# Performance work log

Hardware: AMD Instinct MI355X
Metric: run time of the kernel (lower is better)

## Reference

```python
import jax, jax.numpy as jnp
import numpy as np

B, T, L = 512, 512, 128  # batch, seq_len, tag-vocab size (incl. START=126, STOP=127)


def setup_inputs() -> dict:
    key = jax.random.key(0)
    k1, k2, k3 = jax.random.split(key, 3)
    # scale emissions so exp(gold path score) stays finite in fp32
    feats = jax.random.normal(k1, (B, T, L), dtype=jnp.float32) * 0.05
    # xavier_normal on [L, L] -> std = sqrt(2/(L+L)) = 1/sqrt(L)
    transfer = jax.random.normal(k2, (L, L), dtype=jnp.float32) * (1.0 / np.sqrt(L))
    target = jax.random.randint(k3, (B, T), 0, L - 2, dtype=jnp.int32)
    return {"feats": feats, "transfer": transfer, "target": target,
            "start": L - 2, "stop": L - 1}


def _crf_loss(feats, transfer, target, start, stop):
    # feats: [B, T, L] emissions; transfer: [L, L]; target: [B, T] gold tags
    Bb, Tt, Ll = feats.shape

    # ---- forward algorithm (log-sum-exp DP over tags) ----
    # scores[1] = feats[1] + transfer[start, :]
    prev0 = feats[:, 1] + transfer[start][None, :]  # [B, L]

    def step(prev, f_t):
        # original: scores[t, y] = LSE_x( scores[t-1, x] + feats[t, x] + transfer[x, y] )
        v = prev + f_t                                        # [B, L] over prev-tag x
        new = jax.nn.logsumexp(v[:, :, None] + transfer[None, :, :], axis=1)  # [B, L]
        return new, None

    step = jax.checkpoint(step)  # keep scan residuals to just the carries
    feats_rest = jnp.swapaxes(feats[:, 2:], 0, 1)  # [T-2, B, L]
    prev, _ = jax.lax.scan(step, prev0, feats_rest)
    sentence_score = jax.nn.logsumexp(prev + transfer[:, stop][None, :], axis=1)  # [B]

    # ---- gold path score ----
    emit0 = feats[:, 0, start]  # hh[0, start]
    emit = jnp.take_along_axis(feats[:, 1:], target[:, 1:, None], axis=2)[..., 0].sum(axis=1)
    pre = jnp.concatenate(
        [jnp.full((Bb, 1), start, dtype=target.dtype), target[:, 1:Tt - 1]], axis=1)  # [B, T-1]
    # original reads transfer[pre, tgt].data[0] -> detached constant
    trans = jax.lax.stop_gradient(transfer[pre, target[:, 1:]]).sum(axis=1)
    gold_score = jnp.exp(emit0 + emit + trans)  # original returns torch.exp(score)

    return sentence_score - gold_score  # per-sentence loss, shape [B]


def reference(feats, transfer, target, start, stop):
    return _crf_loss(feats, transfer, target, start, stop)
```

## Files before the change

kernel.cpp:

```cpp
#include <hip/hip_runtime.h>

#define T_DIM 512
#define L_DIM 128

typedef _Float16 h2 __attribute__((ext_vector_type(2)));

#if defined(__has_builtin)
#if __has_builtin(__builtin_amdgcn_fdot2)
#define HAS_FDOT2 1
#endif
#endif

__device__ __forceinline__ float fdot2_acc(h2 a, h2 b, float c) {
#ifdef HAS_FDOT2
    return __builtin_amdgcn_fdot2(a, b, c, false);
#else
    return c + (float)a.x * (float)b.x + (float)a.y * (float)b.y;
#endif
}

__device__ __forceinline__ unsigned int pack_u32(float a, float b) {
    return __builtin_bit_cast(unsigned int, __builtin_amdgcn_cvt_pkrtz(a, b));
}

#define H2C(x) __builtin_bit_cast(h2, (x))

__device__ __forceinline__ void lds_barrier() {
    asm volatile("s_waitcnt lgkmcnt(0)\n\ts_barrier" ::: "memory");
}


#define E_GROUPS(X) X(0) X(1) X(2) X(3) X(4) X(5) X(6) X(7) \
                    X(8) X(9) X(10) X(11) X(12) X(13) X(14) X(15)

__global__ __launch_bounds__(128, 1) void crf_fwd_kernel(
    const float* __restrict__ feats,
    const float* __restrict__ transfer,
    const int* __restrict__ target,
    const int* __restrict__ startp,
    const int* __restrict__ stopp,
    float* __restrict__ out)
{
    __shared__ unsigned int LdsU[2][64] __attribute__((aligned(16)));
    __shared__ float LdsRed[8];

    const int tid  = threadIdx.x;
    const int lane = tid & 63;
    const int wv   = tid >> 6;
    const int g    = tid;
    const int b    = blockIdx.x;
    const int start = startp[0];
    const int stop  = stopp[0];
    const float* fbase = feats + (size_t)b * T_DIM * L_DIM;
    const float LOG128 = 4.852030263919617f;
    const float SCALE  = 0.0078125f;

#define DECL_E(v) uint4 E##v;
    E_GROUPS(DECL_E)
#undef DECL_E

#define LDT(r) transfer[(r) * L_DIM + g]
#define LOAD_E(v) { \
    float e0 = __expf(LDT(8*(v)+0)) * SCALE, e1 = __expf(LDT(8*(v)+1)) * SCALE; \
    float e2 = __expf(LDT(8*(v)+2)) * SCALE, e3 = __expf(LDT(8*(v)+3)) * SCALE; \
    float e4 = __expf(LDT(8*(v)+4)) * SCALE, e5 = __expf(LDT(8*(v)+5)) * SCALE; \
    float e6 = __expf(LDT(8*(v)+6)) * SCALE, e7 = __expf(LDT(8*(v)+7)) * SCALE; \
    E##v.x = pack_u32(e0, e1); E##v.y = pack_u32(e2, e3); \
    E##v.z = pack_u32(e4, e5); E##v.w = pack_u32(e6, e7); }
    E_GROUPS(LOAD_E)
#undef LOAD_E
#undef LDT

    const float trStop = transfer[g * L_DIM + stop];

    {
        float v2 = fbase[1 * L_DIM + g] + fbase[2 * L_DIM + g]
                 + transfer[start * L_DIM + g];
        _Float16 h = (_Float16)__expf(v2);
        reinterpret_cast<unsigned short*>(&LdsU[0][0])[g] =
            __builtin_bit_cast(unsigned short, h);
    }
    float fa = fbase[3 * L_DIM + g];
    float fb = fbase[4 * L_DIM + g];
    float fc = fbase[5 * L_DIM + g];
    float S  = 0.f;
    lds_barrier();

    int cur = 0;
    float accF = 0.f;

    for (int t = 2; t <= T_DIM - 1; ++t) {
        int tp = t + 4; if (tp > T_DIM - 1) tp = T_DIM - 1;
        float fnew = fbase[tp * L_DIM + g];
        float e = __expf(fa);

        if ((t & 15) == 0) {
            h2 h = H2C(LdsU[cur][0]);
            float u0 = (float)h.x;
            e *= 1.0f / u0;
            S += __logf(u0);
        }

        const uint4* U4p = reinterpret_cast<const uint4*>(&LdsU[cur][0]);
        float s0 = 0.f, s1 = 0.f, s2 = 0.f, s3 = 0.f;

#define DOT_G(v, AC) { \
        uint4 p = U4p[v]; \
        AC = fdot2_acc(H2C(p.x), H2C(E##v.x), AC); \
        AC = fdot2_acc(H2C(p.y), H2C(E##v.y), AC); \
        AC = fdot2_acc(H2C(p.z), H2C(E##v.z), AC); \
        AC = fdot2_acc(H2C(p.w), H2C(E##v.w), AC); }

        DOT_G(0,  s0) DOT_G(1,  s1) DOT_G(2,  s2) DOT_G(3,  s3)
        DOT_G(4,  s0) DOT_G(5,  s1) DOT_G(6,  s2) DOT_G(7,  s3)
        DOT_G(8,  s0) DOT_G(9,  s1) DOT_G(10, s2) DOT_G(11, s3)
        DOT_G(12, s0) DOT_G(13, s1) DOT_G(14, s2) DOT_G(15, s3)
#undef DOT_G

        float acc = (s0 + s1) + (s2 + s3);

        if (t < T_DIM - 1) {
            _Float16 h = (_Float16)(acc * e);
            reinterpret_cast<unsigned short*>(&LdsU[cur ^ 1][0])[g] =
                __builtin_bit_cast(unsigned short, h);
            lds_barrier();
            cur ^= 1;
            fa = fb; fb = fc; fc = fnew;
        } else {
            accF = acc;
        }
    }

    S += 510.0f * LOG128;

    float x  = __logf(accF) + S + trStop;
    float mx = x;
#pragma unroll
    for (int d = 1; d < 64; d <<= 1) mx = fmaxf(mx, __shfl_xor(mx, d));
    float ex = __expf(x - mx);
#pragma unroll
    for (int d = 1; d < 64; d <<= 1) ex += __shfl_xor(ex, d);
    if (lane == 0) { LdsRed[wv] = mx; LdsRed[2 + wv] = ex; }

    float es = 0.f, ts = 0.f;
    const int* tgt = target + b * T_DIM;
#pragma unroll
    for (int k = 0; k < 4; ++k) {
        int t = 1 + tid + (k << 7);
        if (t < T_DIM) {
            int tg = tgt[t];
            es += fbase[t * L_DIM + tg];
            int pr = (t == 1) ? start : tgt[t - 1];
            ts += transfer[pr * L_DIM + tg];
        }
    }
#pragma unroll
    for (int d = 1; d < 64; d <<= 1) {
        es += __shfl_xor(es, d);
        ts += __shfl_xor(ts, d);
    }
    if (lane == 0) { LdsRed[4 + wv] = es; LdsRed[6 + wv] = ts; }
    __syncthreads();

    if (tid == 0) {
        float M  = fmaxf(LdsRed[0], LdsRed[1]);
        float Ss = LdsRed[2] * __expf(LdsRed[0] - M)
                 + LdsRed[3] * __expf(LdsRed[1] - M);
        float sentence = M + __logf(Ss);
        float em = LdsRed[4] + LdsRed[5];
        float tn = LdsRed[6] + LdsRed[7];
        float emit0 = fbase[start];
        out[b] = sentence - __expf(emit0 + em + tn);
    }
}

extern "C" void kernel_launch(void* const* d_in, const int* in_sizes, int n_in,
                              void* d_out, int out_size, void* d_ws, size_t ws_size,
                              hipStream_t stream) {
    const float* feats    = (const float*)d_in[0];
    const float* transfer = (const float*)d_in[1];
    const int*   target   = (const int*)d_in[2];
    const int*   startp   = (const int*)d_in[3];
    const int*   stopp    = (const int*)d_in[4];
    float* outp = (float*)d_out;
    int B = in_sizes[0] / (T_DIM * L_DIM);
    hipLaunchKernelGGL(crf_fwd_kernel, dim3(B), dim3(128), 0, stream,
                       feats, transfer, target, startp, stopp, outp);
}
```

Measured before the change: 425.9 us.

## Stage emission rows through double-buffered LDS chunks with vector global loads

```diff
diff --git a/kernel.cpp b/kernel.cpp
--- a/kernel.cpp
+++ b/kernel.cpp
@@ -42,6 +42,7 @@
     float* __restrict__ out)
 {
     __shared__ unsigned int LdsU[2][64] __attribute__((aligned(16)));
+    __shared__ float LdsF[2][16][L_DIM] __attribute__((aligned(16)));
     __shared__ float LdsRed[8];
 
     const int tid  = threadIdx.x;
@@ -54,6 +55,28 @@
     const float* fbase = feats + (size_t)b * T_DIM * L_DIM;
     const float LOG128 = 4.852030263919617f;
     const float SCALE  = 0.0078125f;
+
+    const int srow = tid >> 5;
+    const int scol = (tid & 31) << 2;
+
+    uint4 G0, G1, G2, G3;
+
+#define ISSUE_CHUNK(r0base) { \
+    int rA = (r0base) + srow; \
+    int q0 = rA      > 511 ? 511 : rA; \
+    int q1 = rA + 4  > 511 ? 511 : rA + 4; \
+    int q2 = rA + 8  > 511 ? 511 : rA + 8; \
+    int q3 = rA + 12 > 511 ? 511 : rA + 12; \
+    G0 = *reinterpret_cast<const uint4*>(&fbase[(size_t)q0 * L_DIM + scol]); \
+    G1 = *reinterpret_cast<const uint4*>(&fbase[(size_t)q1 * L_DIM + scol]); \
+    G2 = *reinterpret_cast<const uint4*>(&fbase[(size_t)q2 * L_DIM + scol]); \
+    G3 = *reinterpret_cast<const uint4*>(&fbase[(size_t)q3 * L_DIM + scol]); }
+
+#define WRITE_CHUNK(buf) { \
+    *reinterpret_cast<uint4*>(&LdsF[buf][srow     ][scol]) = G0; \
+    *reinterpret_cast<uint4*>(&LdsF[buf][srow + 4 ][scol]) = G1; \
+    *reinterpret_cast<uint4*>(&LdsF[buf][srow + 8 ][scol]) = G2; \
+    *reinterpret_cast<uint4*>(&LdsF[buf][srow + 12][scol]) = G3; }
 
 #define DECL_E(v) uint4 E##v;
     E_GROUPS(DECL_E)
@@ -80,19 +103,29 @@
         reinterpret_cast<unsigned short*>(&LdsU[0][0])[g] =
             __builtin_bit_cast(unsigned short, h);
     }
-    float fa = fbase[3 * L_DIM + g];
-    float fb = fbase[4 * L_DIM + g];
-    float fc = fbase[5 * L_DIM + g];
-    float S  = 0.f;
+
+    ISSUE_CHUNK(3);
+    WRITE_CHUNK(0);
+    ISSUE_CHUNK(19);
+    float S = 0.f;
     lds_barrier();
 
     int cur = 0;
     float accF = 0.f;
 
     for (int t = 2; t <= T_DIM - 1; ++t) {
-        int tp = t + 4; if (tp > T_DIM - 1) tp = T_DIM - 1;
-        float fnew = fbase[tp * L_DIM + g];
-        float e = __expf(fa);
+        const int s  = (t - 2) & 15;
+        const int k  = (t - 2) >> 4;
+        const int kb = k & 1;
+
+        if (s == 0 && k > 0) {
+            WRITE_CHUNK(kb);
+            if (k < 31) ISSUE_CHUNK(3 + 16 * (k + 1));
+            lds_barrier();
+        }
+
+        float fval = LdsF[kb][s][g];
+        float e = __expf(fval);
 
         if ((t & 15) == 0) {
             h2 h = H2C(LdsU[cur][0]);
@@ -125,7 +158,6 @@
                 __builtin_bit_cast(unsigned short, h);
             lds_barrier();
             cur ^= 1;
-            fa = fb; fb = fc; fc = fnew;
         } else {
             accF = acc;
         }
@@ -145,8 +177,8 @@
     float es = 0.f, ts = 0.f;
     const int* tgt = target + b * T_DIM;
 #pragma unroll
-    for (int k = 0; k < 4; ++k) {
-        int t = 1 + tid + (k << 7);
+    for (int kk = 0; kk < 4; ++kk) {
+        int t = 1 + tid + (kk << 7);
         if (t < T_DIM) {
             int tg = tgt[t];
             es += fbase[t * L_DIM + tg];
```

After: 450.3 us. 1.06x slower.

## Process two batch sequences per block to share barriers and transition registers

Applied to the files above, without the earlier changes.

```diff
diff --git a/kernel.cpp b/kernel.cpp
--- a/kernel.cpp
+++ b/kernel.cpp
@@ -41,17 +41,20 @@
     const int* __restrict__ stopp,
     float* __restrict__ out)
 {
-    __shared__ unsigned int LdsU[2][64] __attribute__((aligned(16)));
-    __shared__ float LdsRed[8];
+    __shared__ unsigned int LdsUA[2][64] __attribute__((aligned(16)));
+    __shared__ unsigned int LdsUB[2][64] __attribute__((aligned(16)));
+    __shared__ float LdsRed[16];
 
     const int tid  = threadIdx.x;
     const int lane = tid & 63;
     const int wv   = tid >> 6;
     const int g    = tid;
-    const int b    = blockIdx.x;
+    const int b0   = blockIdx.x * 2;
+    const int b1   = b0 + 1;
     const int start = startp[0];
     const int stop  = stopp[0];
-    const float* fbase = feats + (size_t)b * T_DIM * L_DIM;
+    const float* fA = feats + (size_t)b0 * T_DIM * L_DIM;
+    const float* fB = feats + (size_t)b1 * T_DIM * L_DIM;
     const float LOG128 = 4.852030263919617f;
     const float SCALE  = 0.0078125f;
 
@@ -74,103 +77,147 @@
     const float trStop = transfer[g * L_DIM + stop];
 
     {
-        float v2 = fbase[1 * L_DIM + g] + fbase[2 * L_DIM + g]
-                 + transfer[start * L_DIM + g];
-        _Float16 h = (_Float16)__expf(v2);
-        reinterpret_cast<unsigned short*>(&LdsU[0][0])[g] =
-            __builtin_bit_cast(unsigned short, h);
-    }
-    float fa = fbase[3 * L_DIM + g];
-    float fb = fbase[4 * L_DIM + g];
-    float fc = fbase[5 * L_DIM + g];
-    float S  = 0.f;
+        float ts0 = transfer[start * L_DIM + g];
+        float vA = fA[1 * L_DIM + g] + fA[2 * L_DIM + g] + ts0;
+        float vB = fB[1 * L_DIM + g] + fB[2 * L_DIM + g] + ts0;
+        _Float16 hA = (_Float16)__expf(vA);
+        _Float16 hB = (_Float16)__expf(vB);
+        reinterpret_cast<unsigned short*>(&LdsUA[0][0])[g] =
+            __builtin_bit_cast(unsigned short, hA);
+        reinterpret_cast<unsigned short*>(&LdsUB[0][0])[g] =
+            __builtin_bit_cast(unsigned short, hB);
+    }
+    float faA = fA[3 * L_DIM + g], faB = fB[3 * L_DIM + g];
+    float fbA = fA[4 * L_DIM + g], fbB = fB[4 * L_DIM + g];
+    float fcA = fA[5 * L_DIM + g], fcB = fB[5 * L_DIM + g];
+    float SA = 0.f, SB = 0.f;
     lds_barrier();
 
     int cur = 0;
-    float accF = 0.f;
+    float accFA = 0.f, accFB = 0.f;
 
     for (int t = 2; t <= T_DIM - 1; ++t) {
         int tp = t + 4; if (tp > T_DIM - 1) tp = T_DIM - 1;
-        float fnew = fbase[tp * L_DIM + g];
-        float e = __expf(fa);
+        float fnA = fA[tp * L_DIM + g];
+        float fnB = fB[tp * L_DIM + g];
+        float eA = __expf(faA);
+        float eB = __expf(faB);
 
         if ((t & 15) == 0) {
-            h2 h = H2C(LdsU[cur][0]);
-            float u0 = (float)h.x;
-            e *= 1.0f / u0;
-            S += __logf(u0);
+            h2 hA = H2C(LdsUA[cur][0]);
+            h2 hB = H2C(LdsUB[cur][0]);
+            float uA = (float)hA.x, uB = (float)hB.x;
+            eA *= 1.0f / uA;  SA += __logf(uA);
+            eB *= 1.0f / uB;  SB += __logf(uB);
         }
 
-        const uint4* U4p = reinterpret_cast<const uint4*>(&LdsU[cur][0]);
+        const uint4* UA = reinterpret_cast<const uint4*>(&LdsUA[cur][0]);
+        const uint4* UB = reinterpret_cast<const uint4*>(&LdsUB[cur][0]);
         float s0 = 0.f, s1 = 0.f, s2 = 0.f, s3 = 0.f;
-
-#define DOT_G(v, AC) { \
-        uint4 p = U4p[v]; \
-        AC = fdot2_acc(H2C(p.x), H2C(E##v.x), AC); \
-        AC = fdot2_acc(H2C(p.y), H2C(E##v.y), AC); \
-        AC = fdot2_acc(H2C(p.z), H2C(E##v.z), AC); \
-        AC = fdot2_acc(H2C(p.w), H2C(E##v.w), AC); }
-
-        DOT_G(0,  s0) DOT_G(1,  s1) DOT_G(2,  s2) DOT_G(3,  s3)
-        DOT_G(4,  s0) DOT_G(5,  s1) DOT_G(6,  s2) DOT_G(7,  s3)
-        DOT_G(8,  s0) DOT_G(9,  s1) DOT_G(10, s2) DOT_G(11, s3)
-        DOT_G(12, s0) DOT_G(13, s1) DOT_G(14, s2) DOT_G(15, s3)
-#undef DOT_G
-
-        float acc = (s0 + s1) + (s2 + s3);
+        float q0 = 0.f, q1 = 0.f, q2 = 0.f, q3 = 0.f;
+
+#define DOT_G2(v, AC, BC) { \
+        uint4 pa = UA[v]; \
+        uint4 pb = UB[v]; \
+        AC = fdot2_acc(H2C(pa.x), H2C(E##v.x), AC); \
+        AC = fdot2_acc(H2C(pa.y), H2C(E##v.y), AC); \
+        AC = fdot2_acc(H2C(pa.z), H2C(E##v.z), AC); \
+        AC = fdot2_acc(H2C(pa.w), H2C(E##v.w), AC); \
+        BC = fdot2_acc(H2C(pb.x), H2C(E##v.x), BC); \
+        BC = fdot2_acc(H2C(pb.y), H2C(E##v.y), BC); \
+        BC = fdot2_acc(H2C(pb.z), H2C(E##v.z), BC); \
+        BC = fdot2_acc(H2C(pb.w), H2C(E##v.w), BC); }
+
+        DOT_G2(0,  s0, q0) DOT_G2(1,  s1, q1) DOT_G2(2,  s2, q2) DOT_G2(3,  s3, q3)
+        DOT_G2(4,  s0, q0) DOT_G2(5,  s1, q1) DOT_G2(6,  s2, q2) DOT_G2(7,  s3, q3)
+        DOT_G2(8,  s0, q0) DOT_G2(9,  s1, q1) DOT_G2(10, s2, q2) DOT_G2(11, s3, q3)
+        DOT_G2(12, s0, q0) DOT_G2(13, s1, q1) DOT_G2(14, s2, q2) DOT_G2(15, s3, q3)
+#undef DOT_G2
+
+        float accA = (s0 + s1) + (s2 + s3);
+        float accB = (q0 + q1) + (q2 + q3);
 
         if (t < T_DIM - 1) {
-            _Float16 h = (_Float16)(acc * e);
-            reinterpret_cast<unsigned short*>(&LdsU[cur ^ 1][0])[g] =
-                __builtin_bit_cast(unsigned short, h);
+            _Float16 hA = (_Float16)(accA * eA);
+            _Float16 hB = (_Float16)(accB * eB);
+            reinterpret_cast<unsigned short*>(&LdsUA[cur ^ 1][0])[g] =
+                __builtin_bit_cast(unsigned short, hA);
+            reinterpret_cast<unsigned short*>(&LdsUB[cur ^ 1][0])[g] =
+                __builtin_bit_cast(unsigned short, hB);
             lds_barrier();
             cur ^= 1;
-            fa = fb; fb = fc; fc = fnew;
+            faA = fbA; fbA = fcA; fcA = fnA;
+            faB = fbB; fbB = fcB; fcB = fnB;
         } else {
-            accF = acc;
+            accFA = accA; accFB = accB;
         }
     }
 
-    S += 510.0f * LOG128;
-
-    float x  = __logf(accF) + S + trStop;
-    float mx = x;
-#pragma unroll
-    for (int d = 1; d < 64; d <<= 1) mx = fmaxf(mx, __shfl_xor(mx, d));
-    float ex = __expf(x - mx);
-#pragma unroll
-    for (int d = 1; d < 64; d <<= 1) ex += __shfl_xor(ex, d);
-    if (lane == 0) { LdsRed[wv] = mx; LdsRed[2 + wv] = ex; }
-
-    float es = 0.f, ts = 0.f;
-    const int* tgt = target + b * T_DIM;
+    SA += 510.0f * LOG128;
+    SB += 510.0f * LOG128;
+
+    float xA = __logf(accFA) + SA + trStop;
+    float xB = __logf(accFB) + SB + trStop;
+    float mA = xA, mB = xB;
+#pragma unroll
+    for (int d = 1; d < 64; d <<= 1) {
+        mA = fmaxf(mA, __shfl_xor(mA, d));
+        mB = fmaxf(mB, __shfl_xor(mB, d));
+    }
+    float eAx = __expf(xA - mA), eBx = __expf(xB - mB);
+#pragma unroll
+    for (int d = 1; d < 64; d <<= 1) {
+        eAx += __shfl_xor(eAx, d);
+        eBx += __shfl_xor(eBx, d);
+    }
+    if (lane == 0) {
+        LdsRed[0 + wv] = mA;  LdsRed[2 + wv] = eAx;
+        LdsRed[8 + wv] = mB;  LdsRed[10 + wv] = eBx;
+    }
+
+    float esA = 0.f, tsA = 0.f, esB = 0.f, tsB = 0.f;
+    const int* tgA = target + b0 * T_DIM;
+    const int* tgB = target + b1 * T_DIM;
 #pragma unroll
     for (int k = 0; k < 4; ++k) {
         int t = 1 + tid + (k << 7);
         if (t < T_DIM) {
-            int tg = tgt[t];
-            es += fbase[t * L_DIM + tg];
-            int pr = (t == 1) ? start : tgt[t - 1];
-            ts += transfer[pr * L_DIM + tg];
+            int a = tgA[t], bb = tgB[t];
+            esA += fA[t * L_DIM + a];
+            esB += fB[t * L_DIM + bb];
+            int pa = (t == 1) ? start : tgA[t - 1];
+            int pb = (t == 1) ? start : tgB[t - 1];
+            tsA += transfer[pa * L_DIM + a];
+            tsB += transfer[pb * L_DIM + bb];
         }
     }
 #pragma unroll
     for (int d = 1; d < 64; d <<= 1) {
-        es += __shfl_xor(es, d);
-        ts += __shfl_xor(ts, d);
-    }
-    if (lane == 0) { LdsRed[4 + wv] = es; LdsRed[6 + wv] = ts; }
+        esA += __shfl_xor(esA, d);  tsA += __shfl_xor(tsA, d);
+        esB += __shfl_xor(esB, d);  tsB += __shfl_xor(tsB, d);
+    }
+    if (lane == 0) {
+        LdsRed[4 + wv]  = esA; LdsRed[6 + wv]  = tsA;
+        LdsRed[12 + wv] = esB; LdsRed[14 + wv] = tsB;
+    }
     __syncthreads();
 
     if (tid == 0) {
-        float M  = fmaxf(LdsRed[0], LdsRed[1]);
-        float Ss = LdsRed[2] * __expf(LdsRed[0] - M)
-                 + LdsRed[3] * __expf(LdsRed[1] - M);
-        float sentence = M + __logf(Ss);
-        float em = LdsRed[4] + LdsRed[5];
-        float tn = LdsRed[6] + LdsRed[7];
-        float emit0 = fbase[start];
-        out[b] = sentence - __expf(emit0 + em + tn);
+        float MA = fmaxf(LdsRed[0], LdsRed[1]);
+        float SsA = LdsRed[2] * __expf(LdsRed[0] - MA)
+                  + LdsRed[3] * __expf(LdsRed[1] - MA);
+        float sentA = MA + __logf(SsA);
+        float emA = LdsRed[4] + LdsRed[5];
+        float tnA = LdsRed[6] + LdsRed[7];
+        out[b0] = sentA - __expf(fA[start] + emA + tnA);
+
+        float MB = fmaxf(LdsRed[8], LdsRed[9]);
+        float SsB = LdsRed[10] * __expf(LdsRed[8] - MB)
+                  + LdsRed[11] * __expf(LdsRed[9] - MB);
+        float sentB = MB + __logf(SsB);
+        float emB = LdsRed[12] + LdsRed[13];
+        float tnB = LdsRed[14] + LdsRed[15];
+        out[b1] = sentB - __expf(fB[start] + emB + tnB);
     }
 }
 
@@ -184,6 +231,6 @@
     const int*   stopp    = (const int*)d_in[4];
     float* outp = (float*)d_out;
     int B = in_sizes[0] / (T_DIM * L_DIM);
-    hipLaunchKernelGGL(crf_fwd_kernel, dim3(B), dim3(128), 0, stream,
+    hipLaunchKernelGGL(crf_fwd_kernel, dim3(B / 2), dim3(128), 0, stream,
                        feats, transfer, target, startp, stopp, outp);
 }
```

New measurement: 738.4 us. +73.4%, slower.
